# Performance work log

Measured on AMD Instinct MI355X. Metric: run time of the kernel, lower is better.

Reference implementation:

```python
import jax, jax.numpy as jnp
import numpy as np

EPS = 1e-8  # torch.nn.CosineSimilarity default eps
V, I, H, L = 50257, 1024, 1024, 16384  # vocab, gru_input_size, gru_hidden_size, max_length


def setup_inputs() -> dict:
    key = jax.random.key(0)
    ks = jax.random.split(key, 12)
    rn = lambda k, shape, s=1.0: jax.random.normal(k, shape, dtype=jnp.float32) * s
    return {
        "token": jax.random.randint(ks[0], (1, 1), 0, V),
        "hidden": rn(ks[1], (1, 1, H)),
        "encoder_outputs": rn(ks[2], (L, H)),
        "emb": rn(ks[3], (V, I)),
        "attn_w": rn(ks[4], (H, I + H), 0.02), "attn_b": jnp.zeros((H,), jnp.float32),
        "comb_w": rn(ks[5], (I, I + H), 0.02), "comb_b": jnp.zeros((I,), jnp.float32),
        "w_ih": rn(ks[6], (3 * H, I), 0.02), "w_hh": rn(ks[7], (3 * H, H), 0.02),
        "b_ih": jnp.zeros((3 * H,), jnp.float32), "b_hh": jnp.zeros((3 * H,), jnp.float32),
        "fc2_w": rn(ks[8], (64, H), 0.02), "fc2_b": jnp.zeros((64,), jnp.float32),
        "out_w": rn(ks[9], (1, 64), 0.02), "out_b": jnp.zeros((1,), jnp.float32),
    }


def reference(token, hidden, encoder_outputs, emb, attn_w, attn_b, comb_w, comb_b,
              w_ih, w_hh, b_ih, b_hh, fc2_w, fc2_b, out_w, out_b):
    # 'identifier'/'keyword' branch; dropout is identity in eval mode.
    embedded = emb[token[0, 0]][None, :]                      # [1, I]
    h0 = hidden[0]                                            # [1, H]
    # attention query projection
    q = jnp.concatenate([embedded, h0], axis=1) @ attn_w.T + attn_b  # [1, H]
    # cosine similarity of q vs each encoder output row (dim=1 broadcast)
    qn = jnp.maximum(jnp.linalg.norm(q[0]), EPS)
    en = jnp.maximum(jnp.linalg.norm(encoder_outputs, axis=1), EPS)  # [L]
    sims = (encoder_outputs @ q[0]) / (qn * en)               # [L]
    attn_weights = jax.nn.softmax(sims)[None, :]              # [1, L]
    attn_applied = attn_weights @ encoder_outputs             # [1, H]
    x = jnp.concatenate([embedded, attn_applied], axis=1) @ comb_w.T + comb_b  # [1, I]
    x = jax.nn.relu(x)
    # single GRU cell step (PyTorch gate convention: r, z, n)
    gi = x @ w_ih.T + b_ih                                    # [1, 3H]
    gh = h0 @ w_hh.T + b_hh                                   # [1, 3H]
    r = jax.nn.sigmoid(gi[:, :H] + gh[:, :H])
    z = jax.nn.sigmoid(gi[:, H:2 * H] + gh[:, H:2 * H])
    n = jnp.tanh(gi[:, 2 * H:] + r * gh[:, 2 * H:])
    h_new = (1.0 - z) * n + z * h0                            # [1, H]
    out = jax.nn.relu(h_new @ fc2_w.T + fc2_b) @ out_w.T + out_b  # [1, 1]
    return out, h_new[None], attn_weights
```

## Files before the change

kernel.cpp:

```cpp
#include <hip/hip_runtime.h>
#include <hip/hip_bf16.h>
#include <math.h>

#define II 1024
#define HH 1024
#define LL 16384
#define EPSF 1e-8f
#define XBLK 64
#define SC_AA 4294967296.0f
#define ISC_AA 2.3283064365386963e-10f
#define SC_GI 4294967296.0f
#define ISC_GI 2.3283064365386963e-10f

typedef unsigned long long ull;

__device__ __forceinline__ float wred_sum(float v) {
    #pragma unroll
    for (int o = 32; o; o >>= 1) v += __shfl_down(v, o);
    return v;
}
__device__ __forceinline__ float wred_sum_all(float v) {
    #pragma unroll
    for (int o = 32; o; o >>= 1) v += __shfl_xor(v, o);
    return v;
}

__global__ __launch_bounds__(256) void n1_kernel(
    const int* __restrict__ token, const float* __restrict__ emb,
    const float* __restrict__ hidden, const float* __restrict__ attn_w,
    const float* __restrict__ attn_b, float* __restrict__ q,
    ull* __restrict__ accs) {
    for (int i = blockIdx.x * 256 + threadIdx.x; i < 10241; i += 65536)
        accs[i] = 0ull;
    int w = (blockIdx.x * blockDim.x + threadIdx.x) >> 6;
    int lane = threadIdx.x & 63;
    const float* er = emb + (size_t)token[0] * II;
    const float* row = attn_w + (size_t)w * (II + HH);
    float acc = 0.f;
    for (int k = lane * 4; k < II + HH; k += 256) {
        float4 w4 = *(const float4*)(row + k);
        const float* src = (k < II) ? (er + k) : (hidden + (k - II));
        float4 x4 = *(const float4*)src;
        acc += w4.x * x4.x + w4.y * x4.y + w4.z * x4.z + w4.w * x4.w;
    }
    acc = wred_sum(acc);
    if (lane == 0) q[w] = acc + attn_b[w];
}

__global__ __launch_bounds__(1024) void n2_kernel(
    const int* __restrict__ token, const float* __restrict__ emb,
    const float* __restrict__ enc, const float* __restrict__ q,
    const float* __restrict__ hidden, const float* __restrict__ w_hh,
    const float* __restrict__ b_hh, const float* __restrict__ comb_w,
    const float* __restrict__ comb_b, float* __restrict__ e_out,
    float* __restrict__ psum, float* __restrict__ gh,
    float* __restrict__ x_emb, ull* __restrict__ aa_int) {
    __shared__ float s_colw[16][1024];
    __shared__ float s_red[16];
    const int b = blockIdx.x, t = threadIdx.x;
    const int wv = t >> 6, lane = t & 63;

    float4 q4[4];
    #pragma unroll
    for (int j = 0; j < 4; ++j) q4[j] = *(const float4*)(q + lane * 4 + j * 256);
    float ss = 0.f;
    #pragma unroll
    for (int j = 0; j < 4; ++j)
        ss += q4[j].x * q4[j].x + q4[j].y * q4[j].y + q4[j].z * q4[j].z +
              q4[j].w * q4[j].w;
    ss = wred_sum_all(ss);
    const float qn = fmaxf(sqrtf(ss), EPSF);

    float cs[16];
    #pragma unroll
    for (int i = 0; i < 16; ++i) cs[i] = 0.f;
    float ewave = 0.f;
    #pragma unroll
    for (int j = 0; j < 4; ++j) {
        int r = b * 64 + wv * 4 + j;
        const float* row = enc + (size_t)r * HH;
        float4 e4[4];
        float dv = 0.f, sv = 0.f;
        #pragma unroll
        for (int k = 0; k < 4; ++k) {
            e4[k] = *(const float4*)(row + lane * 4 + k * 256);
            dv += e4[k].x * q4[k].x + e4[k].y * q4[k].y + e4[k].z * q4[k].z +
                  e4[k].w * q4[k].w;
            sv += e4[k].x * e4[k].x + e4[k].y * e4[k].y + e4[k].z * e4[k].z +
                  e4[k].w * e4[k].w;
        }
        dv = wred_sum_all(dv);
        sv = wred_sum_all(sv);
        float en = fmaxf(sqrtf(sv), EPSF);
        float e = expf(dv / (qn * en) - 1.f);
        if (lane == 0) e_out[r] = e;
        ewave += e;
        #pragma unroll
        for (int k = 0; k < 4; ++k) {
            cs[k * 4 + 0] = fmaf(e, e4[k].x, cs[k * 4 + 0]);
            cs[k * 4 + 1] = fmaf(e, e4[k].y, cs[k * 4 + 1]);
            cs[k * 4 + 2] = fmaf(e, e4[k].z, cs[k * 4 + 2]);
            cs[k * 4 + 3] = fmaf(e, e4[k].w, cs[k * 4 + 3]);
        }
    }
    #pragma unroll
    for (int k = 0; k < 4; ++k)
        *(float4*)&s_colw[wv][k * 256 + lane * 4] = *(float4*)&cs[k * 4];
    if (lane == 0) s_red[wv] = ewave;
    __syncthreads();
    if (wv == 0) {
        float v = (lane < 16) ? s_red[lane] : 0.f;
        v = wred_sum(v);
        if (lane == 0) psum[b] = v;
    }
    {
        float a = 0.f;
        #pragma unroll
        for (int w = 0; w < 16; ++w) a += s_colw[w][t];
        atomicAdd(&aa_int[(b & 3) * 1024 + t],
                  (ull)(long long)llrintf(a * SC_AA));
    }

    if (wv < 12) {
        int r = b * 12 + wv;
        const float* row = w_hh + (size_t)r * HH;
        float acc = 0.f;
        #pragma unroll
        for (int k = lane * 4; k < HH; k += 256) {
            float4 w4 = *(const float4*)(row + k);
            float4 x4 = *(const float4*)(hidden + k);
            acc += w4.x * x4.x + w4.y * x4.y + w4.z * x4.z + w4.w * x4.w;
        }
        acc = wred_sum(acc);
        if (lane == 0) gh[r] = acc + b_hh[r];
    } else {
        int r = b * 4 + (wv - 12);
        const float* row = comb_w + (size_t)r * (II + HH);
        const float* er = emb + (size_t)token[0] * II;
        float acc = 0.f;
        #pragma unroll
        for (int k = lane * 4; k < II; k += 256) {
            float4 w4 = *(const float4*)(row + k);
            float4 x4 = *(const float4*)(er + k);
            acc += w4.x * x4.x + w4.y * x4.y + w4.z * x4.z + w4.w * x4.w;
        }
        acc = wred_sum(acc);
        if (lane == 0) x_emb[r] = acc + comb_b[r];
    }
}

__global__ __launch_bounds__(1024) void n3_kernel(
    const float* __restrict__ comb_w, const float* __restrict__ x_emb,
    const float* __restrict__ w_ih, const float* __restrict__ b_ih,
    const float* __restrict__ gh, const float* __restrict__ hidden,
    const float* __restrict__ fc2_w, const float* __restrict__ fc2_b,
    const float* __restrict__ out_w, const float* __restrict__ out_b,
    const float* __restrict__ e_in, const float* __restrict__ psum,
    const ull* __restrict__ aa_int, ull* __restrict__ gi_acc,
    ull* __restrict__ gc, float* __restrict__ h_new,
    float* __restrict__ out_scalar, float* __restrict__ attn_wout) {
    __shared__ float s_aa[HH];
    __shared__ float s_x[16];
    __shared__ float hsh[HH];
    __shared__ float f[64];
    __shared__ unsigned s_last;
    const int b = blockIdx.x, t = threadIdx.x;
    const int wv = t >> 6, lane = t & 63;

    float4 p4 = *(const float4*)(psum + lane * 4);
    float den = wred_sum_all(p4.x + p4.y + p4.z + p4.w);
    const float inv_den = 1.f / den;

    s_aa[t] = (float)((long long)(aa_int[t] + aa_int[1024 + t] +
                                  aa_int[2048 + t] + aa_int[3072 + t])) *
              ISC_AA * inv_den;
    if (t < 256) {
        int i = b * 256 + t;
        attn_wout[i] = e_in[i] * inv_den;
    }
    {
        float sw = 0.f;
        #pragma unroll
        for (int i = 0; i < 16; ++i) {
            float4 v = *(const float4*)(fc2_w + t * 4 + i * 4096);
            sw += v.x + v.y + v.z + v.w;
        }
        asm volatile("" :: "v"(sw));
    }
    __syncthreads();

    int r = b * 16 + wv;
    {
        const float* row = comb_w + (size_t)r * (II + HH) + II;
        float acc = 0.f;
        #pragma unroll
        for (int k = lane * 4; k < HH; k += 256) {
            float4 w4 = *(const float4*)(row + k);
            acc += w4.x * s_aa[k] + w4.y * s_aa[k + 1] + w4.z * s_aa[k + 2] +
                   w4.w * s_aa[k + 3];
        }
        acc = wred_sum(acc);
        if (lane == 0) s_x[wv] = fmaxf(acc + x_emb[r], 0.f);
    }
    __syncthreads();

    const int c0 = b * 16;
    ull* grep = gi_acc + (size_t)(b & 1) * 3072;
    #pragma unroll
    for (int i = 0; i < 3; ++i) {
        int rr = t + i * 1024;
        const float* wrow = w_ih + (size_t)rr * II + c0;
        float4 w0 = *(const float4*)(wrow + 0);
        float4 w1 = *(const float4*)(wrow + 4);
        float4 w2 = *(const float4*)(wrow + 8);
        float4 w3 = *(const float4*)(wrow + 12);
        float acc = w0.x * s_x[0] + w0.y * s_x[1] + w0.z * s_x[2] +
                    w0.w * s_x[3] + w1.x * s_x[4] + w1.y * s_x[5] +
                    w1.z * s_x[6] + w1.w * s_x[7] + w2.x * s_x[8] +
                    w2.y * s_x[9] + w2.z * s_x[10] + w2.w * s_x[11] +
                    w3.x * s_x[12] + w3.y * s_x[13] + w3.z * s_x[14] +
                    w3.w * s_x[15];
        atomicAdd(&grep[rr], (ull)(long long)llrintf(acc * SC_GI));
    }
    __syncthreads();
    if (t == 0) {
        __threadfence();
        ull old = atomicAdd(gc, 1ull);
        s_last = (old + 1ull == (ull)XBLK) ? 1u : 0u;
    }
    __syncthreads();
    if (!s_last) return;
    __threadfence();

    float gr = (float)((long long)(gi_acc[t] + gi_acc[3072 + t])) * ISC_GI +
               b_ih[t];
    float gz = (float)((long long)(gi_acc[HH + t] + gi_acc[3072 + HH + t])) *
                   ISC_GI + b_ih[HH + t];
    float gn = (float)((long long)(gi_acc[2 * HH + t] +
                                   gi_acc[3072 + 2 * HH + t])) * ISC_GI +
               b_ih[2 * HH + t];
    float rg = 1.f / (1.f + expf(-(gr + gh[t])));
    float zg = 1.f / (1.f + expf(-(gz + gh[HH + t])));
    float ng = tanhf(gn + rg * gh[2 * HH + t]);
    float h = (1.f - zg) * ng + zg * hidden[t];
    hsh[t] = h;
    h_new[t] = h;
    __syncthreads();
    #pragma unroll
    for (int rr2 = 0; rr2 < 4; ++rr2) {
        int r2 = wv * 4 + rr2;
        const float* row = fc2_w + (size_t)r2 * HH;
        float acc = 0.f;
        #pragma unroll
        for (int k = lane * 4; k < HH; k += 256) {
            float4 w4 = *(const float4*)(row + k);
            acc += w4.x * hsh[k] + w4.y * hsh[k + 1] + w4.z * hsh[k + 2] +
                   w4.w * hsh[k + 3];
        }
        acc = wred_sum(acc);
        if (lane == 0) f[r2] = fmaxf(acc + fc2_b[r2], 0.f);
    }
    __syncthreads();
    if (t < 64) {
        float v = f[t] * out_w[t];
        v = wred_sum(v);
        if (t == 0) out_scalar[0] = v + out_b[0];
    }
}

extern "C" void kernel_launch(void* const* d_in, const int* in_sizes, int n_in,
                              void* d_out, int out_size, void* d_ws,
                              size_t ws_size, hipStream_t stream) {
    const int*   token  = (const int*)d_in[0];
    const float* hidden = (const float*)d_in[1];
    const float* enc    = (const float*)d_in[2];
    const float* emb    = (const float*)d_in[3];
    const float* attn_w = (const float*)d_in[4];
    const float* attn_b = (const float*)d_in[5];
    const float* comb_w = (const float*)d_in[6];
    const float* comb_b = (const float*)d_in[7];
    const float* w_ih   = (const float*)d_in[8];
    const float* w_hh   = (const float*)d_in[9];
    const float* b_ih   = (const float*)d_in[10];
    const float* b_hh   = (const float*)d_in[11];
    const float* fc2_w  = (const float*)d_in[12];
    const float* fc2_b  = (const float*)d_in[13];
    const float* out_w  = (const float*)d_in[14];
    const float* out_b  = (const float*)d_in[15];

    float* ws = (float*)d_ws;
    float* q     = ws;
    float* gh    = ws + 1024;
    float* x_emb = ws + 4096;
    float* e     = ws + 5120;
    float* psum  = ws + 21504;
    ull* accs    = (ull*)(ws + 21760);
    ull* aa_int  = accs;
    ull* gi_acc  = accs + 4096;
    ull* gc      = accs + 10240;

    float* out_scalar = (float*)d_out;
    float* h_new      = (float*)d_out + 1;
    float* attn_wout  = (float*)d_out + 1 + HH;

    n1_kernel<<<256, 256, 0, stream>>>(token, emb, hidden, attn_w, attn_b, q,
                                       accs);
    n2_kernel<<<256, 1024, 0, stream>>>(token, emb, enc, q, hidden, w_hh, b_hh,
                                        comb_w, comb_b, e, psum, gh, x_emb,
                                        aa_int);
    n3_kernel<<<XBLK, 1024, 0, stream>>>(comb_w, x_emb, w_ih, b_ih, gh, hidden,
                                         fc2_w, fc2_b, out_w, out_b, e, psum,
                                         aa_int, gi_acc, gc, h_new, out_scalar,
                                         attn_wout);
}
```

Measured before the change: 56.38 us.

## Move gh and x_emb GEMVs into first kernel and rebalance attention grid

The hidden-to-hidden GEMV and the embedding half of the combine GEMV move from the attention kernel into the first kernel, which grows to 1280 blocks so all three projections run in one pass. The attention kernel becomes 512 blocks of 512 threads with two blocks per CU, and its column accumulators spread over 8 replicas instead of 4 to reduce atomic contention. The final kernel uses 32 blocks that each handle 32 combine rows. This shortens the critical path through the attention kernel, in exchange for a larger first kernel and fewer blocks streaming w_ih.

```diff
diff --git a/kernel.cpp b/kernel.cpp
--- a/kernel.cpp
+++ b/kernel.cpp
@@ -6,7 +6,8 @@
 #define HH 1024
 #define LL 16384
 #define EPSF 1e-8f
-#define XBLK 64
+#define XBLK 32
+#define NREP 8
 #define SC_AA 4294967296.0f
 #define ISC_AA 2.3283064365386963e-10f
 #define SC_GI 4294967296.0f
@@ -28,35 +29,62 @@
 __global__ __launch_bounds__(256) void n1_kernel(
     const int* __restrict__ token, const float* __restrict__ emb,
     const float* __restrict__ hidden, const float* __restrict__ attn_w,
-    const float* __restrict__ attn_b, float* __restrict__ q,
+    const float* __restrict__ attn_b, const float* __restrict__ w_hh,
+    const float* __restrict__ b_hh, const float* __restrict__ comb_w,
+    const float* __restrict__ comb_b, float* __restrict__ q,
+    float* __restrict__ gh, float* __restrict__ x_emb,
     ull* __restrict__ accs) {
-    for (int i = blockIdx.x * 256 + threadIdx.x; i < 10241; i += 65536)
-        accs[i] = 0ull;
+    {
+        int i = blockIdx.x * 256 + threadIdx.x;
+        if (i < NREP * 1024 + 2 * 3072 + 1) accs[i] = 0ull;
+    }
     int w = (blockIdx.x * blockDim.x + threadIdx.x) >> 6;
     int lane = threadIdx.x & 63;
     const float* er = emb + (size_t)token[0] * II;
-    const float* row = attn_w + (size_t)w * (II + HH);
-    float acc = 0.f;
-    for (int k = lane * 4; k < II + HH; k += 256) {
-        float4 w4 = *(const float4*)(row + k);
-        const float* src = (k < II) ? (er + k) : (hidden + (k - II));
-        float4 x4 = *(const float4*)src;
-        acc += w4.x * x4.x + w4.y * x4.y + w4.z * x4.z + w4.w * x4.w;
-    }
-    acc = wred_sum(acc);
-    if (lane == 0) q[w] = acc + attn_b[w];
-}
-
-__global__ __launch_bounds__(1024) void n2_kernel(
-    const int* __restrict__ token, const float* __restrict__ emb,
+    if (w < HH) {
+        const float* row = attn_w + (size_t)w * (II + HH);
+        float acc = 0.f;
+        for (int k = lane * 4; k < II + HH; k += 256) {
+            float4 w4 = *(const float4*)(row + k);
+            const float* src = (k < II) ? (er + k) : (hidden + (k - II));
+            float4 x4 = *(const float4*)src;
+            acc += w4.x * x4.x + w4.y * x4.y + w4.z * x4.z + w4.w * x4.w;
+        }
+        acc = wred_sum(acc);
+        if (lane == 0) q[w] = acc + attn_b[w];
+    } else if (w < 4 * HH) {
+        int r = w - HH;
+        const float* row = w_hh + (size_t)r * HH;
+        float acc = 0.f;
+        #pragma unroll
+        for (int k = lane * 4; k < HH; k += 256) {
+            float4 w4 = *(const float4*)(row + k);
+            float4 x4 = *(const float4*)(hidden + k);
+            acc += w4.x * x4.x + w4.y * x4.y + w4.z * x4.z + w4.w * x4.w;
+        }
+        acc = wred_sum(acc);
+        if (lane == 0) gh[r] = acc + b_hh[r];
+    } else {
+        int r = w - 4 * HH;
+        const float* row = comb_w + (size_t)r * (II + HH);
+        float acc = 0.f;
+        #pragma unroll
+        for (int k = lane * 4; k < II; k += 256) {
+            float4 w4 = *(const float4*)(row + k);
+            float4 x4 = *(const float4*)(er + k);
+            acc += w4.x * x4.x + w4.y * x4.y + w4.z * x4.z + w4.w * x4.w;
+        }
+        acc = wred_sum(acc);
+        if (lane == 0) x_emb[r] = acc + comb_b[r];
+    }
+}
+
+__global__ __launch_bounds__(512, 2) void n2_kernel(
     const float* __restrict__ enc, const float* __restrict__ q,
-    const float* __restrict__ hidden, const float* __restrict__ w_hh,
-    const float* __restrict__ b_hh, const float* __restrict__ comb_w,
-    const float* __restrict__ comb_b, float* __restrict__ e_out,
-    float* __restrict__ psum, float* __restrict__ gh,
-    float* __restrict__ x_emb, ull* __restrict__ aa_int) {
-    __shared__ float s_colw[16][1024];
-    __shared__ float s_red[16];
+    float* __restrict__ e_out, float* __restrict__ psum,
+    ull* __restrict__ aa_int) {
+    __shared__ float s_colw[8][1024];
+    __shared__ float s_red[8];
     const int b = blockIdx.x, t = threadIdx.x;
     const int wv = t >> 6, lane = t & 63;
 
@@ -77,7 +105,7 @@
     float ewave = 0.f;
     #pragma unroll
     for (int j = 0; j < 4; ++j) {
-        int r = b * 64 + wv * 4 + j;
+        int r = b * 32 + wv * 4 + j;
         const float* row = enc + (size_t)r * HH;
         float4 e4[4];
         float dv = 0.f, sv = 0.f;
@@ -109,43 +137,20 @@
     if (lane == 0) s_red[wv] = ewave;
     __syncthreads();
     if (wv == 0) {
-        float v = (lane < 16) ? s_red[lane] : 0.f;
+        float v = (lane < 8) ? s_red[lane] : 0.f;
         v = wred_sum(v);
         if (lane == 0) psum[b] = v;
     }
     {
-        float a = 0.f;
-        #pragma unroll
-        for (int w = 0; w < 16; ++w) a += s_colw[w][t];
-        atomicAdd(&aa_int[(b & 3) * 1024 + t],
-                  (ull)(long long)llrintf(a * SC_AA));
-    }
-
-    if (wv < 12) {
-        int r = b * 12 + wv;
-        const float* row = w_hh + (size_t)r * HH;
-        float acc = 0.f;
-        #pragma unroll
-        for (int k = lane * 4; k < HH; k += 256) {
-            float4 w4 = *(const float4*)(row + k);
-            float4 x4 = *(const float4*)(hidden + k);
-            acc += w4.x * x4.x + w4.y * x4.y + w4.z * x4.z + w4.w * x4.w;
-        }
-        acc = wred_sum(acc);
-        if (lane == 0) gh[r] = acc + b_hh[r];
-    } else {
-        int r = b * 4 + (wv - 12);
-        const float* row = comb_w + (size_t)r * (II + HH);
-        const float* er = emb + (size_t)token[0] * II;
-        float acc = 0.f;
-        #pragma unroll
-        for (int k = lane * 4; k < II; k += 256) {
-            float4 w4 = *(const float4*)(row + k);
-            float4 x4 = *(const float4*)(er + k);
-            acc += w4.x * x4.x + w4.y * x4.y + w4.z * x4.z + w4.w * x4.w;
-        }
-        acc = wred_sum(acc);
-        if (lane == 0) x_emb[r] = acc + comb_b[r];
+        float a0 = 0.f, a1 = 0.f;
+        #pragma unroll
+        for (int w = 0; w < 8; ++w) {
+            a0 += s_colw[w][t];
+            a1 += s_colw[w][t + 512];
+        }
+        ull* rep = aa_int + (size_t)(b & (NREP - 1)) * 1024;
+        atomicAdd(&rep[t], (ull)(long long)llrintf(a0 * SC_AA));
+        atomicAdd(&rep[t + 512], (ull)(long long)llrintf(a1 * SC_AA));
     }
 }
 
@@ -160,22 +165,27 @@
     ull* __restrict__ gc, float* __restrict__ h_new,
     float* __restrict__ out_scalar, float* __restrict__ attn_wout) {
     __shared__ float s_aa[HH];
-    __shared__ float s_x[16];
+    __shared__ float s_x[32];
     __shared__ float hsh[HH];
     __shared__ float f[64];
     __shared__ unsigned s_last;
     const int b = blockIdx.x, t = threadIdx.x;
     const int wv = t >> 6, lane = t & 63;
 
-    float4 p4 = *(const float4*)(psum + lane * 4);
-    float den = wred_sum_all(p4.x + p4.y + p4.z + p4.w);
+    float4 p0 = *(const float4*)(psum + lane * 8);
+    float4 p1 = *(const float4*)(psum + lane * 8 + 4);
+    float den = wred_sum_all(p0.x + p0.y + p0.z + p0.w +
+                             p1.x + p1.y + p1.z + p1.w);
     const float inv_den = 1.f / den;
 
-    s_aa[t] = (float)((long long)(aa_int[t] + aa_int[1024 + t] +
-                                  aa_int[2048 + t] + aa_int[3072 + t])) *
-              ISC_AA * inv_den;
-    if (t < 256) {
-        int i = b * 256 + t;
+    {
+        ull s = 0ull;
+        #pragma unroll
+        for (int rep = 0; rep < NREP; ++rep) s += aa_int[rep * 1024 + t];
+        s_aa[t] = (float)((long long)s) * ISC_AA * inv_den;
+    }
+    if (t < 512) {
+        int i = b * 512 + t;
         attn_wout[i] = e_in[i] * inv_den;
     }
     {
@@ -189,8 +199,9 @@
     }
     __syncthreads();
 
-    int r = b * 16 + wv;
-    {
+    #pragma unroll
+    for (int rr = 0; rr < 2; ++rr) {
+        int r = b * 32 + wv * 2 + rr;
         const float* row = comb_w + (size_t)r * (II + HH) + II;
         float acc = 0.f;
         #pragma unroll
@@ -200,26 +211,23 @@
                    w4.w * s_aa[k + 3];
         }
         acc = wred_sum(acc);
-        if (lane == 0) s_x[wv] = fmaxf(acc + x_emb[r], 0.f);
-    }
-    __syncthreads();
-
-    const int c0 = b * 16;
+        if (lane == 0) s_x[wv * 2 + rr] = fmaxf(acc + x_emb[r], 0.f);
+    }
+    __syncthreads();
+
+    const int c0 = b * 32;
     ull* grep = gi_acc + (size_t)(b & 1) * 3072;
     #pragma unroll
     for (int i = 0; i < 3; ++i) {
         int rr = t + i * 1024;
         const float* wrow = w_ih + (size_t)rr * II + c0;
-        float4 w0 = *(const float4*)(wrow + 0);
-        float4 w1 = *(const float4*)(wrow + 4);
-        float4 w2 = *(const float4*)(wrow + 8);
-        float4 w3 = *(const float4*)(wrow + 12);
-        float acc = w0.x * s_x[0] + w0.y * s_x[1] + w0.z * s_x[2] +
-                    w0.w * s_x[3] + w1.x * s_x[4] + w1.y * s_x[5] +
-                    w1.z * s_x[6] + w1.w * s_x[7] + w2.x * s_x[8] +
-                    w2.y * s_x[9] + w2.z * s_x[10] + w2.w * s_x[11] +
-                    w3.x * s_x[12] + w3.y * s_x[13] + w3.z * s_x[14] +
-                    w3.w * s_x[15];
+        float acc = 0.f;
+        #pragma unroll
+        for (int k = 0; k < 8; ++k) {
+            float4 w4 = *(const float4*)(wrow + k * 4);
+            acc += w4.x * s_x[k * 4 + 0] + w4.y * s_x[k * 4 + 1] +
+                   w4.z * s_x[k * 4 + 2] + w4.w * s_x[k * 4 + 3];
+        }
         atomicAdd(&grep[rr], (ull)(long long)llrintf(acc * SC_GI));
     }
     __syncthreads();
@@ -294,20 +302,19 @@
     float* x_emb = ws + 4096;
     float* e     = ws + 5120;
     float* psum  = ws + 21504;
-    ull* accs    = (ull*)(ws + 21760);
+    ull* accs    = (ull*)(ws + 22016);
     ull* aa_int  = accs;
-    ull* gi_acc  = accs + 4096;
-    ull* gc      = accs + 10240;
+    ull* gi_acc  = accs + 8192;
+    ull* gc      = accs + 14336;
 
     float* out_scalar = (float*)d_out;
     float* h_new      = (float*)d_out + 1;
     float* attn_wout  = (float*)d_out + 1 + HH;
 
-    n1_kernel<<<256, 256, 0, stream>>>(token, emb, hidden, attn_w, attn_b, q,
-                                       accs);
-    n2_kernel<<<256, 1024, 0, stream>>>(token, emb, enc, q, hidden, w_hh, b_hh,
-                                        comb_w, comb_b, e, psum, gh, x_emb,
-                                        aa_int);
+    n1_kernel<<<1280, 256, 0, stream>>>(token, emb, hidden, attn_w, attn_b,
+                                        w_hh, b_hh, comb_w, comb_b, q, gh,
+                                        x_emb, accs);
+    n2_kernel<<<512, 512, 0, stream>>>(enc, q, e, psum, aa_int);
     n3_kernel<<<XBLK, 1024, 0, stream>>>(comb_w, x_emb, w_ih, b_ih, gh, hidden,
                                          fc2_w, fc2_b, out_w, out_b, e, psum,
                                          aa_int, gi_acc, gc, h_new, out_scalar,
```

New measurement: 61.07 us. 1.08x slower.
